# Kernel optimization log

Hardware: AMD Instinct MI355X
Metric: run time of the kernel (lower is better)

The kernel has to match this reference:

```python
import jax, jax.numpy as jnp
import numpy as np

N_NODES = 500000
N_EDGES = 8000000
LEN_SCALE = 20000.0


def setup_inputs() -> dict:
    key = jax.random.key(0)
    ks = jax.random.split(key, 10)
    inp = {
        'read_length': jax.random.randint(ks[0], (N_NODES,), 0, 20000, dtype=jnp.int64)
        if jax.config.read('jax_enable_x64') else jax.random.randint(ks[0], (N_NODES,), 0, 20000, dtype=jnp.int32),
        'edge_index': jax.random.randint(ks[1], (2, N_EDGES), 0, N_NODES, dtype=jnp.int32),
    }
    dims = [1, 4, 8, 16, 32]
    for i in range(4):
        fan_in, fan_out = dims[i], dims[i + 1]
        inp[f'W{i+1}'] = jax.random.normal(ks[2 + 2 * i], (fan_in, fan_out), jnp.float32) / np.sqrt(fan_in)
        inp[f'b{i+1}'] = jax.random.normal(ks[3 + 2 * i], (fan_out,), jnp.float32) * 0.01
    return inp


def _gcn_conv(x, W, b, src, dst, norm_e, dinv):
    # PyG GCNConv: linear first, then D^-1/2 (A+I) D^-1/2 aggregation, then bias.
    xw = x @ W                                              # [N, F_out]
    msg = xw[src] * norm_e[:, None]                         # [E, F_out]
    agg = jax.ops.segment_sum(msg, dst, num_segments=x.shape[0])
    # self-loop term handled analytically: norm for (i,i) is deg_i^-1
    return agg + xw * dinv[:, None] + b


def reference(read_length, edge_index, W1, b1, W2, b2, W3, b3, W4, b4):
    src, dst = edge_index[0], edge_index[1]
    # x = read_length / 20000, unsqueezed to [N, 1]
    x = (read_length.astype(jnp.float32) / LEN_SCALE)[:, None]
    N = x.shape[0]
    # degree with self-loops (edge weight 1)
    deg = jax.ops.segment_sum(jnp.ones_like(src, dtype=jnp.float32), dst, num_segments=N) + 1.0
    dinv_sqrt = jax.lax.rsqrt(deg)
    dinv = 1.0 / deg
    norm_e = dinv_sqrt[src] * dinv_sqrt[dst]                # [E]
    x = _gcn_conv(x, W1, b1, src, dst, norm_e, dinv)
    x = _gcn_conv(x, W2, b2, src, dst, norm_e, dinv)
    x = _gcn_conv(x, W3, b3, src, dst, norm_e, dinv)
    x = _gcn_conv(x, W4, b4, src, dst, norm_e, dinv)
    return x
```

## Files before the change

### kernel.cpp

```cpp
#include <hip/hip_runtime.h>
#include <hip/hip_bf16.h>


#define BLK  256
#define SBLK 1024
#define NB   512
#define BSH  10
#define PB   512
#define BUFCAP 15872
#define BUF2 17920
#define CAP  18432

__global__ void probe_i64(const int* __restrict__ rl32, int* __restrict__ flag,
                          int* __restrict__ cur) {
    __shared__ int sm[BLK];
    int t = threadIdx.x;
    if (blockIdx.x == 1) {
        for (int k = t; k < NB; k += BLK) cur[k] = 0;
        return;
    }
    int acc = 0;
    for (int k = t; k < 1024; k += blockDim.x)
        acc |= rl32[2 * k + 1];
    sm[t] = acc; __syncthreads();
    for (int off = BLK / 2; off > 0; off >>= 1) {
        if (t < off) sm[t] |= sm[t + off];
        __syncthreads();
    }
    if (t == 0) *flag = (sm[0] != 0) ? 1 : 0;
}

__global__ __launch_bounds__(SBLK)
void scatter(const int* __restrict__ src, const int* __restrict__ dst,
             int* __restrict__ cur, unsigned* __restrict__ epart, int E) {
    __shared__ unsigned buf[BUFCAP];
    __shared__ int h[NB];
    __shared__ int c0[NB];
    __shared__ int gpos[NB];
    __shared__ int wsum[8];
    int j = blockIdx.x, t = threadIdx.x;
    int lane = t & 63, w = t >> 6;
    int chunk = (E + PB - 1) / PB;
    int beg = j * chunk, end = min(beg + chunk, E);
    for (int s = beg; s < end; s += BUFCAP) {
        int se = min(s + BUFCAP, end);
        for (int b = t; b < NB; b += SBLK) h[b] = 0;
        __syncthreads();
        for (int e = s + t; e < se; e += SBLK)
            atomicAdd(&h[((unsigned)dst[e]) >> BSH], 1);
        __syncthreads();
        if (t < NB) {
            int v = h[t];
            int run = v;
#pragma unroll
            for (int off = 1; off < 64; off <<= 1) {
                int u = __shfl_up(run, off);
                if (lane >= off) run += u;
            }
            if (lane == 63) wsum[w] = run;
            c0[t] = run - v;
        }
        __syncthreads();
        if (t < 8) {
            int v = wsum[t];
            int run = v;
#pragma unroll
            for (int off = 1; off < 8; off <<= 1) {
                int u = __shfl_up(run, off, 8);
                if ((t & 7) >= off) run += u;
            }
            wsum[t] = run - v;
        }
        __syncthreads();
        if (t < NB) c0[t] += wsum[w];
        __syncthreads();
        for (int e = s + t; e < se; e += SBLK) {
            unsigned d = (unsigned)dst[e];
            int b = d >> BSH;
            int slot = atomicAdd(&c0[b], 1);
            buf[slot] = ((d & 1023u) << 19) | (unsigned)src[e];
        }
        __syncthreads();
        if (t < NB) {
            int n = h[t];
            gpos[t] = (n > 0) ? atomicAdd(&cur[t], n) : 0;
        }
        __syncthreads();
        for (int b = w; b < NB; b += (SBLK >> 6)) {
            int n = h[b];
            int lo = c0[b] - n;
            int gp = gpos[b];
            int left = CAP - gp;
            if (left < 0) left = 0;
            if (n > left) n = left;
            unsigned gb = (unsigned)b * CAP + (unsigned)gp;
            for (int k = lane; k < n; k += 64)
                epart[gb + k] = buf[lo + k];
        }
        __syncthreads();
    }
}

__global__ __launch_bounds__(1024)
void csr_init(const unsigned* __restrict__ epart, const int* __restrict__ cur,
              const int* __restrict__ rl, const int* __restrict__ flag,
              unsigned* __restrict__ epart2, int* __restrict__ bstart,
              float* __restrict__ dinv, float2* __restrict__ v0, int N,
              const float* __restrict__ W1, const float* __restrict__ b1,
              const float* __restrict__ W2, const float* __restrict__ b2,
              const float* __restrict__ W3, const float* __restrict__ b3,
              const float* __restrict__ W4, const float* __restrict__ b4,
              float* __restrict__ c, int seg) {
    __shared__ unsigned buf[BUF2];
    __shared__ int sc[1024];
    __shared__ int cu[1024];
    __shared__ int wsum[16];
    __shared__ int s_beg, s_n;
    int b = blockIdx.x, t = threadIdx.x;
    if (b == gridDim.x - 1) {
        __shared__ float p3[16], q3[16], r3[16];
        if (t == 0) {
            float p2[8], q2[8];
            for (int j = 0; j < 8; ++j) {
                float s1 = 0.f, s2 = 0.f;
                for (int k = 0; k < 4; ++k) {
                    float w = W2[k * 8 + j];
                    s1 += W1[k] * w;
                    s2 += b1[k] * w;
                }
                p2[j] = s1; q2[j] = s2;
            }
            for (int m = 0; m < 16; ++m) {
                float s1 = 0.f, s2 = 0.f, s3 = 0.f;
                for (int j = 0; j < 8; ++j) {
                    float w = W3[j * 16 + m];
                    s1 += p2[j] * w; s2 += q2[j] * w;
                    s3 += b2[j] * w;
                }
                p3[m] = s1; q3[m] = s2; r3[m] = s3;
            }
        }
        __syncthreads();
        if (t < 32) {
            float c4 = 0.f, c3 = 0.f, c2 = 0.f, c1 = 0.f;
            for (int k = 0; k < 16; ++k) {
                float w = W4[k * 32 + t];
                c4 += p3[k] * w; c3 += q3[k] * w; c2 += r3[k] * w;
                c1 += b3[k] * w;
            }
            c[t] = c4; c[32 + t] = c3; c[64 + t] = c2; c[96 + t] = c1;
        }
        return;
    }
    int lane = t & 63, w = t >> 6;
    if (t < 64) {
        int pre = 0, nn = 0;
        for (int k = t; k < NB; k += 64) {
            int v = min(cur[k], CAP);
            if (k < b) pre += v;
            if (k == b) nn = v;
        }
        for (int off = 1; off < 64; off <<= 1) {
            pre += __shfl_xor(pre, off);
            nn  += __shfl_xor(nn, off);
        }
        if (t == 0) { s_beg = pre; s_n = nn; }
    }
    sc[t] = 0;
    __syncthreads();
    int n = s_n;
    int gseg = b * CAP;
    int beg = seg ? gseg : s_beg;
    if (t == 0) bstart[b] = beg;
    if (b == gridDim.x - 2 && t == 1) bstart[b + 1] = beg + n;
    for (int e = t; e < n; e += 1024)
        atomicAdd(&sc[epart[gseg + e] >> 19], 1);
    __syncthreads();
    int v = sc[t];
    int run = v;
#pragma unroll
    for (int off = 1; off < 64; off <<= 1) {
        int u = __shfl_up(run, off);
        if (lane >= off) run += u;
    }
    if (lane == 63) wsum[w] = run;
    __syncthreads();
    if (t < 16) {
        int vv = wsum[t];
        int r2 = vv;
#pragma unroll
        for (int off = 1; off < 16; off <<= 1) {
            int u = __shfl_up(r2, off, 16);
            if ((t & 15) >= off) r2 += u;
        }
        wsum[t] = r2 - vv;
    }
    __syncthreads();
    int incl = run + wsum[w];
    int start = incl - v;
    cu[t] = start;
    int gi = (b << 10) + t;
    if (gi < N) {
        int rv = (*flag) ? rl[gi] : rl[2 * gi];
        float d = (float)v + 1.0f;
        dinv[gi] = 1.0f / d;
        float rs = rsqrtf(d);
        float2 u; u.x = rs * ((float)rv * (1.0f / 20000.0f)); u.y = rs;
        v0[gi] = u;
    }
    __syncthreads();
    if (n <= BUF2) {
        for (int e = t; e < n; e += 1024) {
            unsigned p = epart[gseg + e];
            int slot = atomicAdd(&cu[p >> 19], 1);
            buf[slot] = p;
        }
        __syncthreads();
        for (int k = t; k < n; k += 1024)
            epart2[beg + k] = buf[k];
    } else if (!seg) {
        for (int e = t; e < n; e += 1024) {
            unsigned p = epart[gseg + e];
            int slot = atomicAdd(&cu[p >> 19], 1);
            epart2[beg + slot] = p;
        }
    }
}

__global__ __launch_bounds__(1024)
void gather_seg(const unsigned* __restrict__ ep, const int* __restrict__ bstart,
                const int* __restrict__ cur, int seg,
                const float2* __restrict__ vin, float2* __restrict__ vout,
                const float* __restrict__ dinv, float* __restrict__ zsave, int N) {
    __shared__ float ax[1024];
    __shared__ float ay[1024];
    int b = blockIdx.x, t = threadIdx.x;
    ax[t] = 0.f; ay[t] = 0.f;
    __syncthreads();
    int beg = bstart[b];
    int n = seg ? min(cur[b], CAP) : (bstart[b + 1] - beg);
    int end = beg + n;
    int lane = t & 63, sub = lane & 15;
    for (int base = beg + (t - lane); base < end; base += 1024) {
        int e = base + lane;
        unsigned p = (e < end) ? ep[e] : 0xFFFFFFFFu;
        int key = (int)(p >> 19);
        float vx = 0.f, vy = 0.f;
        if (e < end) {
            float2 u = vin[p & 0x7FFFFu];
            vx = u.x; vy = u.y;
        }
#pragma unroll
        for (int off = 1; off < 16; off <<= 1) {
            float ox = __shfl_up(vx, off, 16);
            float oy = __shfl_up(vy, off, 16);
            int ok = __shfl_up(key, off, 16);
            bool act = (sub >= off) && (ok == key);
            vx += act ? ox : 0.f;
            vy += act ? oy : 0.f;
        }
        int nk = __shfl_down(key, 1);
        bool tail = (sub == 15) || (lane == 63) || (nk != key);
        if (tail && key < 1024) {
            atomicAdd(&ax[key], vx);
            atomicAdd(&ay[key], vy);
        }
    }
    __syncthreads();
    int gi = (b << 10) + t;
    if (gi < N) {
        float2 self = vin[gi];
        float di = dinv[gi];
        float2 o; o.x = (ax[t] + self.x) * di; o.y = (ay[t] + self.y) * di;
        vout[gi] = o;
        if (zsave) zsave[gi] = o.y;
    }
}

__global__ __launch_bounds__(1024)
void gather_out_seg(const unsigned* __restrict__ ep, const int* __restrict__ bstart,
                    const float2* __restrict__ vin, const float* __restrict__ dinv,
                    const float* __restrict__ z1, const float* __restrict__ z2,
                    const float* __restrict__ z3, const float* __restrict__ c,
                    const float* __restrict__ b4, float* __restrict__ out, int N) {
    __shared__ float ax[1024];
    __shared__ float sqs[1024];
    int b = blockIdx.x, t = threadIdx.x;
    ax[t] = 0.f;
    __syncthreads();
    int beg = bstart[b], end = bstart[b + 1];
    int lane = t & 63, sub = lane & 15;
    for (int base = beg + (t - lane); base < end; base += 1024) {
        int e = base + lane;
        unsigned p = (e < end) ? ep[e] : 0xFFFFFFFFu;
        int key = (int)(p >> 19);
        float vx = 0.f;
        if (e < end) vx = vin[p & 0x7FFFFu].x;
#pragma unroll
        for (int off = 1; off < 16; off <<= 1) {
            float ox = __shfl_up(vx, off, 16);
            int ok = __shfl_up(key, off, 16);
            bool act = (sub >= off) && (ok == key);
            vx += act ? ox : 0.f;
        }
        int nk = __shfl_down(key, 1);
        bool tail = (sub == 15) || (lane == 63) || (nk != key);
        if (tail && key < 1024) atomicAdd(&ax[key], vx);
    }
    __syncthreads();
    int gi = (b << 10) + t;
    float ox = 0.f, sq = 0.f;
    if (gi < N) {
        float di = dinv[gi];
        ox = (ax[t] + vin[gi].x) * di;
        sq = rsqrtf(di);
    }
    __syncthreads();
    ax[t] = ox; sqs[t] = sq;
    __syncthreads();
    int f = t & 31, half = t >> 5;
    float c4 = c[f], c3 = c[32 + f], c2 = c[64 + f], c1 = c[96 + f], bb = b4[f];
    int base_node = b << 10;
    for (int p = 0; p < 32; ++p) {
        int ln = p * 32 + half;
        int g = base_node + ln;
        if (g < N) {
            float zz1 = z1[g], zz2 = z2[g], zz3 = z3[g];
            float val = sqs[ln] * (ax[ln] * c4 + zz3 * c3 + zz2 * c2 + zz1 * c1) + bb;
            out[(size_t)g * 32 + f] = val;
        }
    }
}

__global__ void write_out(const float2* __restrict__ v0, const float* __restrict__ z1,
                          const float* __restrict__ z2, const float* __restrict__ z3,
                          const float* __restrict__ dinv, const float* __restrict__ c,
                          const float* __restrict__ b4,
                          float* __restrict__ out, int N) {
    int t = blockIdx.x * blockDim.x + threadIdx.x;
    int i = t >> 5, f = t & 31;
    if (i < N) {
        float sq = rsqrtf(dinv[i]);
        float v = sq * (v0[i].x * c[f] + z3[i] * c[32 + f] + z2[i] * c[64 + f]
                        + z1[i] * c[96 + f])
                  + b4[f];
        out[(size_t)i * 32 + f] = v;
    }
}

extern "C" void kernel_launch(void* const* d_in, const int* in_sizes, int n_in,
                              void* d_out, int out_size, void* d_ws, size_t ws_size,
                              hipStream_t stream) {
    const int N = in_sizes[0];
    const int E = in_sizes[1] / 2;
    const int* rl  = (const int*)d_in[0];
    const int* src = (const int*)d_in[1];
    const int* dst = src + E;
    const float* W1 = (const float*)d_in[2];
    const float* b1 = (const float*)d_in[3];
    const float* W2 = (const float*)d_in[4];
    const float* b2 = (const float*)d_in[5];
    const float* W3 = (const float*)d_in[6];
    const float* b3 = (const float*)d_in[7];
    const float* W4 = (const float*)d_in[8];
    const float* b4 = (const float*)d_in[9];

    const int gbNode = (N + 1023) / 1024;

    char* w = (char*)d_ws;
    float2* v0   = (float2*)w;                w += (size_t)N * 8;
    float2* v1   = (float2*)w;                w += (size_t)N * 8;
    float*  dinv = (float*)w;                 w += (size_t)N * 4;
    float*  z1   = (float*)w;                 w += (size_t)N * 4;
    float*  z2   = (float*)w;                 w += (size_t)N * 4;
    float*  z3   = (float*)w;                 w += (size_t)N * 4;
    int*    bstart = (int*)w;                 w += (NB + 1) * 4;
    int*    cur  = (int*)w;                   w += NB * 4;
    float*  c    = (float*)w;                 w += 128 * 4;
    int*    flag = (int*)w;                   w += 16;
    size_t used = (size_t)(w - (char*)d_ws);
    used = (used + 255) & ~(size_t)255;
    bool fits = (used + (size_t)E * 4) <= ws_size;
    unsigned* epart  = (unsigned*)d_out;
    unsigned* epart2 = fits ? (unsigned*)((char*)d_ws + used) : epart;
    const int seg = fits ? 0 : 1;

    probe_i64<<<2, BLK, 0, stream>>>(rl, flag, cur);

    scatter<<<PB, SBLK, 0, stream>>>(src, dst, cur, epart, E);

    csr_init<<<gbNode + 1, 1024, 0, stream>>>(epart, cur, rl, flag, epart2, bstart,
                                              dinv, v0, N,
                                              W1, b1, W2, b2, W3, b3, W4, b4, c, seg);

    gather_seg<<<gbNode, 1024, 0, stream>>>(epart2, bstart, cur, seg, v0, v1, dinv, z1, N);
    gather_seg<<<gbNode, 1024, 0, stream>>>(epart2, bstart, cur, seg, v1, v0, dinv, z2, N);
    gather_seg<<<gbNode, 1024, 0, stream>>>(epart2, bstart, cur, seg, v0, v1, dinv, z3, N);
    if (fits) {
        gather_out_seg<<<gbNode, 1024, 0, stream>>>(epart2, bstart, v1, dinv,
                                                    z1, z2, z3, c, b4,
                                                    (float*)d_out, N);
    } else {
        gather_seg<<<gbNode, 1024, 0, stream>>>(epart2, bstart, cur, seg, v1, v0, dinv,
                                                (float*)nullptr, N);
        write_out<<<(N * 32 + BLK - 1) / BLK, BLK, 0, stream>>>(
            v0, z1, z2, z3, dinv, c, b4, (float*)d_out, N);
    }
}
```

Measured before the change: 383.2 us.

## Fuse four GCN sweeps into one cooperative kernel with grid syncs

Replaces the four separate gather launches with a single cooperative kernel that runs all propagation sweeps, separated by grid-wide barriers, and writes the final 32-wide output in place. The probe kernel is folded into an extra scatter block, and the counter reset becomes a memset. The aim is to remove launch gaps and tail effects between dependent sweeps. It requires all 489 blocks of 1024 threads to be co-resident, and it falls back to the old path if the cooperative launch fails.

```diff
diff --git a/kernel.cpp b/kernel.cpp
--- a/kernel.cpp
+++ b/kernel.cpp
@@ -1,5 +1,7 @@
 #include <hip/hip_runtime.h>
-#include <hip/hip_bf16.h>
+#include <hip/hip_cooperative_groups.h>
+
+namespace cg = cooperative_groups;
 
 
 #define BLK  256
@@ -11,35 +13,30 @@
 #define BUF2 17920
 #define CAP  18432
 
-__global__ void probe_i64(const int* __restrict__ rl32, int* __restrict__ flag,
-                          int* __restrict__ cur) {
-    __shared__ int sm[BLK];
-    int t = threadIdx.x;
-    if (blockIdx.x == 1) {
-        for (int k = t; k < NB; k += BLK) cur[k] = 0;
-        return;
-    }
-    int acc = 0;
-    for (int k = t; k < 1024; k += blockDim.x)
-        acc |= rl32[2 * k + 1];
-    sm[t] = acc; __syncthreads();
-    for (int off = BLK / 2; off > 0; off >>= 1) {
-        if (t < off) sm[t] |= sm[t + off];
-        __syncthreads();
-    }
-    if (t == 0) *flag = (sm[0] != 0) ? 1 : 0;
-}
-
 __global__ __launch_bounds__(SBLK)
 void scatter(const int* __restrict__ src, const int* __restrict__ dst,
-             int* __restrict__ cur, unsigned* __restrict__ epart, int E) {
+             int* __restrict__ cur, unsigned* __restrict__ epart, int E,
+             const int* __restrict__ rl32, int* __restrict__ flag) {
     __shared__ unsigned buf[BUFCAP];
     __shared__ int h[NB];
     __shared__ int c0[NB];
     __shared__ int gpos[NB];
-    __shared__ int wsum[8];
+    __shared__ int wsum[16];
     int j = blockIdx.x, t = threadIdx.x;
     int lane = t & 63, w = t >> 6;
+    if (j == PB) {
+        int acc = rl32[2 * t + 1];
+#pragma unroll
+        for (int off = 1; off < 64; off <<= 1) acc |= __shfl_xor(acc, off);
+        if (lane == 0) h[w] = acc;
+        __syncthreads();
+        if (t == 0) {
+            int a = 0;
+            for (int i = 0; i < 16; ++i) a |= h[i];
+            *flag = (a != 0) ? 1 : 0;
+        }
+        return;
+    }
     int chunk = (E + PB - 1) / PB;
     int beg = j * chunk, end = min(beg + chunk, E);
     for (int s = beg; s < end; s += BUFCAP) {
@@ -227,6 +224,112 @@
     }
 }
 
+__device__ __forceinline__ void sweep_xy(const unsigned* __restrict__ ep,
+    int beg, int end, int t, int lane, int sub, int gi, int N,
+    const float2* __restrict__ vin, float2* __restrict__ vout,
+    const float* __restrict__ dinv, float* __restrict__ zsave,
+    float* ax, float* ay) {
+    ax[t] = 0.f; ay[t] = 0.f;
+    __syncthreads();
+    for (int base = beg + (t - lane); base < end; base += 1024) {
+        int e = base + lane;
+        unsigned p = (e < end) ? ep[e] : 0xFFFFFFFFu;
+        int key = (int)(p >> 19);
+        float vx = 0.f, vy = 0.f;
+        if (e < end) {
+            float2 u = vin[p & 0x7FFFFu];
+            vx = u.x; vy = u.y;
+        }
+#pragma unroll
+        for (int off = 1; off < 16; off <<= 1) {
+            float ox = __shfl_up(vx, off, 16);
+            float oy = __shfl_up(vy, off, 16);
+            int ok = __shfl_up(key, off, 16);
+            bool act = (sub >= off) && (ok == key);
+            vx += act ? ox : 0.f;
+            vy += act ? oy : 0.f;
+        }
+        int nk = __shfl_down(key, 1);
+        bool tail = (sub == 15) || (lane == 63) || (nk != key);
+        if (tail && key < 1024) {
+            atomicAdd(&ax[key], vx);
+            atomicAdd(&ay[key], vy);
+        }
+    }
+    __syncthreads();
+    if (gi < N) {
+        float2 self = vin[gi];
+        float di = dinv[gi];
+        float2 o; o.x = (ax[t] + self.x) * di; o.y = (ay[t] + self.y) * di;
+        vout[gi] = o;
+        zsave[gi] = o.y;
+    }
+}
+
+__global__ __launch_bounds__(1024, 8)
+void sweeps_coop(const unsigned* __restrict__ ep, const int* __restrict__ bstart,
+                 float2* __restrict__ v0, float2* __restrict__ v1,
+                 const float* __restrict__ dinv,
+                 float* __restrict__ z1, float* __restrict__ z2,
+                 float* __restrict__ z3, const float* __restrict__ c,
+                 const float* __restrict__ b4, float* __restrict__ out, int N) {
+    __shared__ float ax[1024];
+    __shared__ float ay[1024];
+    cg::grid_group grid = cg::this_grid();
+    int b = blockIdx.x, t = threadIdx.x;
+    int lane = t & 63, sub = lane & 15;
+    int beg = bstart[b], end = bstart[b + 1];
+    int gi = (b << 10) + t;
+    sweep_xy(ep, beg, end, t, lane, sub, gi, N, v0, v1, dinv, z1, ax, ay);
+    __threadfence(); grid.sync();
+    sweep_xy(ep, beg, end, t, lane, sub, gi, N, v1, v0, dinv, z2, ax, ay);
+    __threadfence(); grid.sync();
+    sweep_xy(ep, beg, end, t, lane, sub, gi, N, v0, v1, dinv, z3, ax, ay);
+    __threadfence(); grid.sync();
+    ax[t] = 0.f;
+    __syncthreads();
+    for (int base = beg + (t - lane); base < end; base += 1024) {
+        int e = base + lane;
+        unsigned p = (e < end) ? ep[e] : 0xFFFFFFFFu;
+        int key = (int)(p >> 19);
+        float vx = 0.f;
+        if (e < end) vx = v1[p & 0x7FFFFu].x;
+#pragma unroll
+        for (int off = 1; off < 16; off <<= 1) {
+            float ox = __shfl_up(vx, off, 16);
+            int ok = __shfl_up(key, off, 16);
+            bool act = (sub >= off) && (ok == key);
+            vx += act ? ox : 0.f;
+        }
+        int nk = __shfl_down(key, 1);
+        bool tail = (sub == 15) || (lane == 63) || (nk != key);
+        if (tail && key < 1024) atomicAdd(&ax[key], vx);
+    }
+    __syncthreads();
+    float ox = 0.f, sq = 0.f;
+    if (gi < N) {
+        float di = dinv[gi];
+        ox = (ax[t] + v1[gi].x) * di;
+        sq = rsqrtf(di);
+    }
+    __syncthreads();
+    ax[t] = ox; ay[t] = sq;
+    __syncthreads();
+    int f = t & 31, half = t >> 5;
+    float c4 = c[f], c3 = c[32 + f], c2 = c[64 + f], c1 = c[96 + f], bb = b4[f];
+    int base_node = b << 10;
+    for (int p = 0; p < 32; ++p) {
+        int ln = p * 32 + half;
+        int g = base_node + ln;
+        if (g < N) {
+            float zz1 = z1[g], zz2 = z2[g], zz3 = z3[g];
+            float val = ay[ln] * (ax[ln] * c4 + zz3 * c3 + zz2 * c2 + zz1 * c1) + bb;
+            out[(size_t)g * 32 + f] = val;
+        }
+    }
+}
+
+
 __global__ __launch_bounds__(1024)
 void gather_seg(const unsigned* __restrict__ ep, const int* __restrict__ bstart,
                 const int* __restrict__ cur, int seg,
@@ -385,25 +488,43 @@
     unsigned* epart2 = fits ? (unsigned*)((char*)d_ws + used) : epart;
     const int seg = fits ? 0 : 1;
 
-    probe_i64<<<2, BLK, 0, stream>>>(rl, flag, cur);
-
-    scatter<<<PB, SBLK, 0, stream>>>(src, dst, cur, epart, E);
+    hipMemsetAsync(cur, 0, NB * sizeof(int), stream);
+
+    scatter<<<PB + 1, SBLK, 0, stream>>>(src, dst, cur, epart, E, rl, flag);
 
     csr_init<<<gbNode + 1, 1024, 0, stream>>>(epart, cur, rl, flag, epart2, bstart,
                                               dinv, v0, N,
                                               W1, b1, W2, b2, W3, b3, W4, b4, c, seg);
 
-    gather_seg<<<gbNode, 1024, 0, stream>>>(epart2, bstart, cur, seg, v0, v1, dinv, z1, N);
-    gather_seg<<<gbNode, 1024, 0, stream>>>(epart2, bstart, cur, seg, v1, v0, dinv, z2, N);
-    gather_seg<<<gbNode, 1024, 0, stream>>>(epart2, bstart, cur, seg, v0, v1, dinv, z3, N);
+    bool done = false;
     if (fits) {
-        gather_out_seg<<<gbNode, 1024, 0, stream>>>(epart2, bstart, v1, dinv,
-                                                    z1, z2, z3, c, b4,
-                                                    (float*)d_out, N);
-    } else {
-        gather_seg<<<gbNode, 1024, 0, stream>>>(epart2, bstart, cur, seg, v1, v0, dinv,
-                                                (float*)nullptr, N);
-        write_out<<<(N * 32 + BLK - 1) / BLK, BLK, 0, stream>>>(
-            v0, z1, z2, z3, dinv, c, b4, (float*)d_out, N);
-    }
-}
+        float* outp = (float*)d_out;
+        int Nv = N;
+        void* args[] = { (void*)&epart2, (void*)&bstart, (void*)&v0, (void*)&v1,
+                         (void*)&dinv, (void*)&z1, (void*)&z2, (void*)&z3,
+                         (void*)&c, (void*)&b4, (void*)&outp, (void*)&Nv };
+        hipError_t err = hipLaunchCooperativeKernel((void*)sweeps_coop,
+                                                    dim3(gbNode), dim3(1024),
+                                                    args, 0, stream);
+        if (err == hipSuccess) {
+            done = true;
+        } else {
+            (void)hipGetLastError();
+        }
+    }
+    if (!done) {
+        gather_seg<<<gbNode, 1024, 0, stream>>>(epart2, bstart, cur, seg, v0, v1, dinv, z1, N);
+        gather_seg<<<gbNode, 1024, 0, stream>>>(epart2, bstart, cur, seg, v1, v0, dinv, z2, N);
+        gather_seg<<<gbNode, 1024, 0, stream>>>(epart2, bstart, cur, seg, v0, v1, dinv, z3, N);
+        if (fits) {
+            gather_out_seg<<<gbNode, 1024, 0, stream>>>(epart2, bstart, v1, dinv,
+                                                        z1, z2, z3, c, b4,
+                                                        (float*)d_out, N);
+        } else {
+            gather_seg<<<gbNode, 1024, 0, stream>>>(epart2, bstart, cur, seg, v1, v0, dinv,
+                                                    (float*)nullptr, N);
+            write_out<<<(N * 32 + BLK - 1) / BLK, BLK, 0, stream>>>(
+                v0, z1, z2, z3, dinv, c, b4, (float*)d_out, N);
+        }
+    }
+}
```

After: 1.067 ms. +178.4%, slower.
